# Performance work log

Hardware: AMD Instinct MI355X
Metric: run time of the kernel (lower is better)

## Reference

```python
import jax, jax.numpy as jnp
import numpy as np

B, Q, T, C = 2, 300, 25, 256
NH, NL, NP = 8, 4, 4
DFF = 1024
HD = C // NH
SHAPES = [(128, 128), (64, 64), (32, 32), (16, 16)]  # (H_l, W_l) per level
S = sum(h * w for h, w in SHAPES)
LQ = Q * T


def setup_inputs() -> dict:
    key = jax.random.key(0)
    ks = jax.random.split(key, 16)
    rn = lambda k, shape, s=0.02: jax.random.normal(k, shape, jnp.float32) * s
    starts = np.cumsum([0] + [h * w for h, w in SHAPES[:-1]])
    return {
        "tgt_text": jax.random.normal(ks[0], (B, Q, T, C), jnp.float32),
        "query_pos_text": jax.random.normal(ks[1], (B, Q, T, C), jnp.float32),
        "reference_points": jax.random.uniform(ks[2], (B, LQ, NL, 2), jnp.float32),
        "src": jax.random.normal(ks[3], (B, S, C), jnp.float32),
        "src_spatial_shapes": jnp.array(SHAPES, jnp.int32),
        "level_start_index": jnp.array(starts, jnp.int32),
        "in_proj_w": rn(ks[4], (3 * C, C)), "in_proj_b": jnp.zeros((3 * C,), jnp.float32),
        "out_proj_w": rn(ks[5], (C, C)), "out_proj_b": jnp.zeros((C,), jnp.float32),
        "ln1_g": jnp.ones((C,), jnp.float32), "ln1_b": jnp.zeros((C,), jnp.float32),
        "samp_off_w": rn(ks[6], (NH * NL * NP * 2, C)), "samp_off_b": rn(ks[7], (NH * NL * NP * 2,), 0.5),
        "aw_w": rn(ks[8], (NH * NL * NP, C)), "aw_b": jnp.zeros((NH * NL * NP,), jnp.float32),
        "vp_w": rn(ks[9], (C, C)), "vp_b": jnp.zeros((C,), jnp.float32),
        "op_w": rn(ks[10], (C, C)), "op_b": jnp.zeros((C,), jnp.float32),
        "ln2_g": jnp.ones((C,), jnp.float32), "ln2_b": jnp.zeros((C,), jnp.float32),
        "ffn1_w": rn(ks[11], (DFF, C)), "ffn1_b": jnp.zeros((DFF,), jnp.float32),
        "ffn2_w": rn(ks[12], (C, DFF)), "ffn2_b": jnp.zeros((C,), jnp.float32),
        "ln3_g": jnp.ones((C,), jnp.float32), "ln3_b": jnp.zeros((C,), jnp.float32),
    }


def _ln(x, g, b):
    m = jnp.mean(x, axis=-1, keepdims=True)
    v = jnp.var(x, axis=-1, keepdims=True)
    return (x - m) / jnp.sqrt(v + 1e-5) * g + b


def _self_attn(tgt, pos, in_proj_w, in_proj_b, out_proj_w, out_proj_b):
    # torch nn.MultiheadAttention math: q,k carry pos, v is raw tgt
    qk = (tgt + pos).reshape(B * Q, T, C)
    x = tgt.reshape(B * Q, T, C)
    Wq, Wk, Wv = jnp.split(in_proj_w, 3, axis=0)
    bq, bk, bv = jnp.split(in_proj_b, 3, axis=0)
    heads = lambda t: t.reshape(B * Q, T, NH, HD).transpose(0, 2, 1, 3)
    q = heads(qk @ Wq.T + bq)
    k = heads(qk @ Wk.T + bk)
    v = heads(x @ Wv.T + bv)
    attn = jax.nn.softmax(jnp.einsum("bhqd,bhkd->bhqk", q, k) / jnp.sqrt(jnp.float32(HD)), axis=-1)
    o = jnp.einsum("bhqk,bhkd->bhqd", attn, v).transpose(0, 2, 1, 3).reshape(B * Q, T, C)
    return (o @ out_proj_w.T + out_proj_b).reshape(B, Q, T, C)


def _ms_deform_attn(query, reference_points, src, shapes, samp_off_w, samp_off_b, aw_w, aw_b, vp_w, vp_b, op_w, op_b):
    # query: [B, LQ, C]; src: [B, S, C]
    value = (src @ vp_w.T + vp_b).reshape(B, S, NH, HD)
    off = (query @ samp_off_w.T + samp_off_b).reshape(B, LQ, NH, NL, NP, 2)
    aw = jax.nn.softmax((query @ aw_w.T + aw_b).reshape(B, LQ, NH, NL * NP), axis=-1)
    aw = aw.reshape(B, LQ, NH, NL, NP)
    # normalizer is (W_l, H_l)
    norm = jnp.array([[w, h] for (h, w) in shapes], jnp.float32)
    loc = reference_points[:, :, None, :, None, :] + off / norm[None, None, None, :, None, :]
    starts = np.cumsum([0] + [h * w for h, w in shapes])
    accum = jnp.zeros((B, NH, LQ, HD), jnp.float32)
    for l, (Hl, Wl) in enumerate(shapes):
        vl = value[:, starts[l]:starts[l] + Hl * Wl].transpose(0, 2, 1, 3)  # [B,NH,HW,HD]
        # grid_sample align_corners=False pixel coords
        xl = (loc[:, :, :, l, :, 0] * Wl - 0.5).transpose(0, 2, 1, 3).reshape(B, NH, LQ * NP)
        yl = (loc[:, :, :, l, :, 1] * Hl - 0.5).transpose(0, 2, 1, 3).reshape(B, NH, LQ * NP)
        x0 = jnp.floor(xl); y0 = jnp.floor(yl)
        wx1 = xl - x0; wy1 = yl - y0
        x0i = x0.astype(jnp.int32); y0i = y0.astype(jnp.int32)
        samp = jnp.zeros((B, NH, LQ * NP, HD), jnp.float32)
        for dx, dy, w in ((0, 0, (1 - wx1) * (1 - wy1)), (1, 0, wx1 * (1 - wy1)),
                          (0, 1, (1 - wx1) * wy1), (1, 1, wx1 * wy1)):
            xi = x0i + dx; yi = y0i + dy
            valid = (xi >= 0) & (xi < Wl) & (yi >= 0) & (yi < Hl)
            lin = jnp.clip(yi, 0, Hl - 1) * Wl + jnp.clip(xi, 0, Wl - 1)
            g = jnp.take_along_axis(vl, lin[..., None], axis=2)  # [B,NH,LQ*NP,HD]
            samp = samp + g * (w * valid)[..., None]
        samp = samp.reshape(B, NH, LQ, NP, HD)
        awl = aw[:, :, :, l, :].transpose(0, 2, 1, 3)  # [B,NH,LQ,NP]
        accum = accum + jnp.sum(samp * awl[..., None], axis=3)
    out = accum.transpose(0, 2, 1, 3).reshape(B, LQ, C)
    return out @ op_w.T + op_b


def reference(tgt_text, query_pos_text, reference_points, src, src_spatial_shapes, level_start_index,
              in_proj_w, in_proj_b, out_proj_w, out_proj_b, ln1_g, ln1_b,
              samp_off_w, samp_off_b, aw_w, aw_b, vp_w, vp_b, op_w, op_b, ln2_g, ln2_b,
              ffn1_w, ffn1_b, ffn2_w, ffn2_b, ln3_g, ln3_b):
    shapes = [tuple(int(v) for v in row) for row in np.asarray(src_spatial_shapes)]  # static
    # --- intra-text self-attention ---
    tgt2 = _self_attn(tgt_text, query_pos_text, in_proj_w, in_proj_b, out_proj_w, out_proj_b)
    tgt = _ln(tgt_text + tgt2, ln1_g, ln1_b)
    # --- multi-scale deformable cross-attention ---
    query = (tgt + query_pos_text).reshape(B, LQ, C)
    cross = _ms_deform_attn(query, reference_points, src, shapes,
                            samp_off_w, samp_off_b, aw_w, aw_b, vp_w, vp_b, op_w, op_b)
    tgt = _ln(tgt + cross.reshape(B, Q, T, C), ln2_g, ln2_b)
    # --- FFN ---
    ffn = jax.nn.relu(tgt @ ffn1_w.T + ffn1_b) @ ffn2_w.T + ffn2_b
    return _ln(tgt + ffn, ln3_g, ln3_b)
```

## Files before the change

### kernel.cpp

```cpp
#include <hip/hip_runtime.h>
#include <cstddef>

#define B_ 2
#define Q_ 300
#define T_ 25
#define C_ 256
#define NH_ 8
#define NL_ 4
#define NP_ 4
#define HD_ 32
#define DFF_ 1024
#define LQ_ (Q_ * T_)
#define NTOK_ (B_ * LQ_)
#define S_ 21760
#define BS_ (B_ * S_)

typedef __bf16 bf16x8 __attribute__((ext_vector_type(8)));
typedef float floatx4 __attribute__((ext_vector_type(4)));
typedef unsigned short ushort_t;

__device__ __forceinline__ unsigned pack_bf16(float x, float y) {
    unsigned ux = __float_as_uint(x) + 0x8000u;
    unsigned uy = __float_as_uint(y) + 0x8000u;
    return (ux >> 16) | (uy & 0xFFFF0000u);
}
__device__ __forceinline__ ushort_t f2bf_s(float x) {
    return (ushort_t)((__float_as_uint(x) + 0x8000u) >> 16);
}
__device__ __forceinline__ float bf2f(ushort_t u) {
    return __uint_as_float((unsigned)u << 16);
}

#define WOFF_IP   0
#define WOFF_OUT  196608
#define WOFF_VP   262144
#define WOFF_SO   327680
#define WOFF_AW   393216
#define WOFF_OP   425984
#define WOFF_F1   491520
#define WOFF_F2   753664
#define WTOTAL    1015808

__global__ __launch_bounds__(256) void convw_kernel(
    const float* __restrict__ ipw, const float* __restrict__ outw,
    const float* __restrict__ vpw, const float* __restrict__ sampw,
    const float* __restrict__ aww, const float* __restrict__ opw,
    const float* __restrict__ f1w, const float* __restrict__ f2w,
    ushort_t* __restrict__ dst)
{
    long long g = ((long long)blockIdx.x * 256 + threadIdx.x) * 8;
    if (g >= WTOTAL) return;
    const float* src; long long off;
    if      (g < WOFF_OUT) { src = ipw;   off = WOFF_IP; }
    else if (g < WOFF_VP)  { src = outw;  off = WOFF_OUT; }
    else if (g < WOFF_SO)  { src = vpw;   off = WOFF_VP; }
    else if (g < WOFF_AW)  { src = sampw; off = WOFF_SO; }
    else if (g < WOFF_OP)  { src = aww;   off = WOFF_AW; }
    else if (g < WOFF_F1)  { src = opw;   off = WOFF_OP; }
    else if (g < WOFF_F2)  { src = f1w;   off = WOFF_F1; }
    else                   { src = f2w;   off = WOFF_F2; }
    const float4* s4 = (const float4*)(src + (g - off));
    float4 a = s4[0], b = s4[1];
    uint4 o;
    o.x = pack_bf16(a.x, a.y); o.y = pack_bf16(a.z, a.w);
    o.z = pack_bf16(b.x, b.y); o.w = pack_bf16(b.z, b.w);
    *(uint4*)(dst + g) = o;
}

#define GBN 128
#define GBK 64
#define LDA_S 72

template<int AMODE, int OUTMODE, int GBMT>
__global__ __launch_bounds__(256) void gemm_w(
    const void* __restrict__ Av, const float* __restrict__ A2,
    const ushort_t* __restrict__ W,
    const float* __restrict__ bias, const float* __restrict__ bias2, int N1,
    void* __restrict__ Cv, long long partStride,
    int M, int N, int K, int kChunk, int ldc, int relu)
{
    constexpr int LA = GBMT / 16;
    constexpr int LB = 8;
    constexpr int WM = GBMT / 2;
    constexpr int NI = WM / 16;

    __shared__ unsigned short Asl[GBMT * LDA_S];
    __shared__ unsigned short Bsl[GBN * LDA_S];

    const int m0 = blockIdx.x * GBMT;
    if (m0 >= M) return;
    const int n0 = blockIdx.y * GBN;
    const int z  = blockIdx.z;
    const int kbeg = z * kChunk;
    const int kend = min(K, kbeg + kChunk);

    const int t  = threadIdx.x;
    const int wid  = t >> 6;
    const int lane = t & 63;
    const int wm = (wid >> 1) * WM;
    const int wn = (wid & 1) * 64;
    const int fm = lane & 15;
    const int fq = (lane >> 4) * 8;

    const bool addA2 = (AMODE == 1) && (n0 < N1);

    floatx4 acc[NI][4];
    #pragma unroll
    for (int i = 0; i < NI; ++i)
        #pragma unroll
        for (int j = 0; j < 4; ++j)
            acc[i][j] = (floatx4){0.f, 0.f, 0.f, 0.f};

    float4 pa[LA];
    uint2  pab[LA];
    uint2  pwb[LB];
    const float* Af = (const float*)Av;
    const ushort_t* Ab = (const ushort_t*)Av;

    auto load_tiles = [&](int k0) {
        #pragma unroll
        for (int i = 0; i < LA; ++i) {
            int idx = t + 256 * i;
            int row = idx >> 4;
            int c4  = (idx & 15) * 4;
            int gm = m0 + row;
            if constexpr (AMODE == 2) {
                uint2 v = {0u, 0u};
                if (gm < M) v = *(const uint2*)(Ab + (size_t)gm * K + k0 + c4);
                pab[i] = v;
            } else {
                float4 v = make_float4(0.f, 0.f, 0.f, 0.f);
                if (gm < M) {
                    v = *(const float4*)(Af + (size_t)gm * K + k0 + c4);
                    if constexpr (AMODE == 1) {
                        if (addA2) {
                            float4 v2 = *(const float4*)(A2 + (size_t)gm * K + k0 + c4);
                            v.x += v2.x; v.y += v2.y; v.z += v2.z; v.w += v2.w;
                        }
                    }
                }
                pa[i] = v;
            }
        }
        #pragma unroll
        for (int i = 0; i < LB; ++i) {
            int idx = t + 256 * i;
            int row = idx >> 4;
            int c4  = (idx & 15) * 4;
            pwb[i] = *(const uint2*)(W + (size_t)(n0 + row) * K + k0 + c4);
        }
    };

    load_tiles(kbeg);
    for (int k0 = kbeg; k0 < kend; k0 += GBK) {
        #pragma unroll
        for (int i = 0; i < LA; ++i) {
            int idx = t + 256 * i;
            int row = idx >> 4;
            int c4  = (idx & 15) * 4;
            if constexpr (AMODE == 2) {
                *(uint2*)&Asl[row * LDA_S + c4] = pab[i];
            } else {
                uint2 p;
                p.x = pack_bf16(pa[i].x, pa[i].y);
                p.y = pack_bf16(pa[i].z, pa[i].w);
                *(uint2*)&Asl[row * LDA_S + c4] = p;
            }
        }
        #pragma unroll
        for (int i = 0; i < LB; ++i) {
            int idx = t + 256 * i;
            int row = idx >> 4;
            int c4  = (idx & 15) * 4;
            *(uint2*)&Bsl[row * LDA_S + c4] = pwb[i];
        }
        if (k0 + GBK < kend) load_tiles(k0 + GBK);
        __syncthreads();

        #pragma unroll
        for (int kk = 0; kk < 2; ++kk) {
            bf16x8 af[NI], bfr[4];
            #pragma unroll
            for (int i = 0; i < NI; ++i)
                af[i] = *(const bf16x8*)&Asl[(wm + i * 16 + fm) * LDA_S + kk * 32 + fq];
            #pragma unroll
            for (int j = 0; j < 4; ++j)
                bfr[j] = *(const bf16x8*)&Bsl[(wn + j * 16 + fm) * LDA_S + kk * 32 + fq];

            #pragma unroll
            for (int i = 0; i < NI; ++i)
                #pragma unroll
                for (int j = 0; j < 4; ++j)
                    acc[i][j] = __builtin_amdgcn_mfma_f32_16x16x32_bf16(af[i], bfr[j], acc[i][j], 0, 0, 0);
        }
        __syncthreads();
    }

    float* Cf = (float*)Cv + (long long)z * partStride;
    ushort_t* Cb = (ushort_t*)Cv;
    const int cr = (lane >> 4) * 4;
    const int cc = lane & 15;
    #pragma unroll
    for (int j = 0; j < 4; ++j) {
        int gn = n0 + wn + j * 16 + cc;
        float bia = 0.f;
        if (z == 0) bia = (bias2 && gn >= N1) ? bias2[gn - N1] : bias[gn];
        #pragma unroll
        for (int i = 0; i < NI; ++i) {
            #pragma unroll
            for (int r = 0; r < 4; ++r) {
                int gm = m0 + wm + i * 16 + cr + r;
                if (gm < M) {
                    float v = acc[i][j][r] + bia;
                    if (relu) v = fmaxf(v, 0.f);
                    if constexpr (OUTMODE == 2) {
                        int bb = gm >= S_;
                        int s  = gm - bb * S_;
                        Cb[(((size_t)(bb * 8 + (gn >> 5))) * S_ + s) * 32 + (gn & 31)] = f2bf_s(v);
                    } else if constexpr (OUTMODE == 1) {
                        Cb[(size_t)gm * ldc + gn] = f2bf_s(v);
                    } else {
                        Cf[(size_t)gm * ldc + gn] = v;
                    }
                }
            }
        }
    }
}

__global__ __launch_bounds__(64) void attn_kernel(
    const ushort_t* __restrict__ qkv,
    ushort_t* __restrict__ o)
{
    int sh = blockIdx.x;
    int s = sh >> 3, h = sh & 7;
    __shared__ float qs[T_][HD_], ks[T_][HD_], vs[T_][HD_];
    int t = threadIdx.x;

    for (int idx = t; idx < T_ * HD_; idx += 64) {
        int i = idx >> 5, d = idx & 31;
        size_t base = ((size_t)(s * T_ + i)) * 768 + h * HD_ + d;
        qs[i][d] = bf2f(qkv[base]);
        ks[i][d] = bf2f(qkv[base + 256]);
        vs[i][d] = bf2f(qkv[base + 512]);
    }
    __syncthreads();

    if (t < T_) {
        float sc[T_];
        float mx = -1e30f;
        #pragma unroll
        for (int j = 0; j < T_; ++j) {
            float dot = 0.f;
            #pragma unroll
            for (int d = 0; d < HD_; ++d) dot += qs[t][d] * ks[j][d];
            sc[j] = dot * 0.17677669529663687f;
            mx = fmaxf(mx, sc[j]);
        }
        float sum = 0.f;
        #pragma unroll
        for (int j = 0; j < T_; ++j) { sc[j] = __expf(sc[j] - mx); sum += sc[j]; }
        float inv = 1.f / sum;
        float out[HD_];
        #pragma unroll
        for (int d = 0; d < HD_; ++d) out[d] = 0.f;
        for (int j = 0; j < T_; ++j) {
            float p = sc[j] * inv;
            #pragma unroll
            for (int d = 0; d < HD_; ++d) out[d] += p * vs[j][d];
        }
        size_t ob = ((size_t)(s * T_ + t)) * C_ + h * HD_;
        #pragma unroll
        for (int d = 0; d < HD_; ++d) o[ob + d] = f2bf_s(out[d]);
    }
}

__global__ __launch_bounds__(256) void ln4_kernel(
    const float* __restrict__ x, const float* __restrict__ r,
    int nparts, long long rstride,
    const float* __restrict__ g, const float* __restrict__ b,
    float* __restrict__ out, const float* __restrict__ pos,
    float* __restrict__ qout)
{
    const int wave = threadIdx.x >> 6;
    const int lane = threadIdx.x & 63;
    const int tok = blockIdx.x * 4 + wave;
    const size_t base = (size_t)tok * C_ + lane * 4;

    float4 v = *(const float4*)(x + base);
    for (int p = 0; p < nparts; ++p) {
        float4 rv = *(const float4*)(r + base + (long long)p * rstride);
        v.x += rv.x; v.y += rv.y; v.z += rv.z; v.w += rv.w;
    }
    float s  = v.x + v.y + v.z + v.w;
    float ss = v.x * v.x + v.y * v.y + v.z * v.z + v.w * v.w;
    #pragma unroll
    for (int m = 32; m; m >>= 1) {
        s  += __shfl_xor(s, m);
        ss += __shfl_xor(ss, m);
    }
    float mean = s * (1.f / 256.f);
    float var  = ss * (1.f / 256.f) - mean * mean;
    float rstd = rsqrtf(var + 1e-5f);

    float4 gv = *(const float4*)(g + lane * 4);
    float4 bv = *(const float4*)(b + lane * 4);
    float4 y;
    y.x = (v.x - mean) * rstd * gv.x + bv.x;
    y.y = (v.y - mean) * rstd * gv.y + bv.y;
    y.z = (v.z - mean) * rstd * gv.z + bv.z;
    y.w = (v.w - mean) * rstd * gv.w + bv.w;
    *(float4*)(out + base) = y;
    if (qout) {
        float4 pv = *(const float4*)(pos + base);
        float4 q;
        q.x = y.x + pv.x; q.y = y.y + pv.y; q.z = y.z + pv.z; q.w = y.w + pv.w;
        *(float4*)(qout + base) = q;
    }
}

#define DCHUNK_ 118
__global__ __launch_bounds__(256) void deform_kernel(
    const ushort_t* __restrict__ value,
    const float* __restrict__ d12,
    const float* __restrict__ refpts,
    ushort_t* __restrict__ out)
{
    const int bi    = blockIdx.x;
    const int xcd   = bi & 7;
    const int yy    = bi >> 3;
    const int combo = xcd + 8 * (yy & 1);
    const int chunk = yy >> 1;
    const int h     = combo & 7;
    const int b     = combo >> 3;

    __shared__ float tls[64][60];

    const int tid = threadIdx.x;
    const int t0  = chunk * 64;

    #pragma unroll
    for (int i = 0; i < 2; ++i) {
        int idx  = tid + 256 * i;
        int trow = idx >> 3;
        int c4   = (idx & 7) * 4;
        int tl   = min(t0 + trow, LQ_ - 1);
        float4 v;
        v.x = __builtin_nontemporal_load(d12 + (size_t)(b * LQ_ + tl) * 384 + h * 32 + c4 + 0);
        v.y = __builtin_nontemporal_load(d12 + (size_t)(b * LQ_ + tl) * 384 + h * 32 + c4 + 1);
        v.z = __builtin_nontemporal_load(d12 + (size_t)(b * LQ_ + tl) * 384 + h * 32 + c4 + 2);
        v.w = __builtin_nontemporal_load(d12 + (size_t)(b * LQ_ + tl) * 384 + h * 32 + c4 + 3);
        *(float4*)&tls[trow][c4] = v;
    }
    {
        int trow = tid >> 2;
        int c4   = (tid & 3) * 4;
        int tl   = min(t0 + trow, LQ_ - 1);
        float4 v;
        v.x = __builtin_nontemporal_load(d12 + (size_t)(b * LQ_ + tl) * 384 + 256 + h * 16 + c4 + 0);
        v.y = __builtin_nontemporal_load(d12 + (size_t)(b * LQ_ + tl) * 384 + 256 + h * 16 + c4 + 1);
        v.z = __builtin_nontemporal_load(d12 + (size_t)(b * LQ_ + tl) * 384 + 256 + h * 16 + c4 + 2);
        v.w = __builtin_nontemporal_load(d12 + (size_t)(b * LQ_ + tl) * 384 + 256 + h * 16 + c4 + 3);
        *(float4*)&tls[trow][32 + c4] = v;
    }
    if (tid < 128) {
        int trow = tid >> 1;
        int c4   = (tid & 1) * 4;
        int tl   = min(t0 + trow, LQ_ - 1);
        float4 v;
        v.x = __builtin_nontemporal_load(refpts + (size_t)(b * LQ_ + tl) * 8 + c4 + 0);
        v.y = __builtin_nontemporal_load(refpts + (size_t)(b * LQ_ + tl) * 8 + c4 + 1);
        v.z = __builtin_nontemporal_load(refpts + (size_t)(b * LQ_ + tl) * 8 + c4 + 2);
        v.w = __builtin_nontemporal_load(refpts + (size_t)(b * LQ_ + tl) * 8 + c4 + 3);
        *(float4*)&tls[trow][48 + c4] = v;
    }
    __syncthreads();

    if (tid < 64) {
        float lg[16];
        float mx = -1e30f;
        #pragma unroll
        for (int i = 0; i < 16; ++i) { lg[i] = tls[tid][32 + i]; mx = fmaxf(mx, lg[i]); }
        float sum = 0.f;
        #pragma unroll
        for (int i = 0; i < 16; ++i) { lg[i] = __expf(lg[i] - mx); sum += lg[i]; }
        float inv = 1.f / sum;
        #pragma unroll
        for (int i = 0; i < 16; ++i) tls[tid][32 + i] = lg[i] * inv;
    }
    __syncthreads();

    const int wave = tid >> 6;
    const int lane = tid & 63;
    const int ti   = lane >> 2;
    const int d8   = (lane & 3) * 8;
    const int row  = wave * 16 + ti;

    int tl = t0 + row;
    const bool active = (tl < LQ_);
    tl = min(tl, LQ_ - 1);
    const int tok = b * LQ_ + tl;

    const int HW[4]     = {128, 64, 32, 16};
    const int starts[4] = {0, 16384, 20480, 21504};

    const ushort_t* vplane = value + (size_t)combo * ((size_t)S_ * HD_) + d8;
    const float* trow = tls[row];

    float accv[8];
    #pragma unroll
    for (int i = 0; i < 8; ++i) accv[i] = 0.f;

    #pragma unroll
    for (int l = 0; l < 4; ++l) {
        const int Hl = HW[l], Wl = HW[l];
        float rx = trow[48 + l * 2 + 0];
        float ry = trow[48 + l * 2 + 1];
        const ushort_t* vbase = vplane + (size_t)starts[l] * HD_;
        #pragma unroll
        for (int p = 0; p < 4; ++p) {
            float ox = trow[l * 8 + p * 2 + 0];
            float oy = trow[l * 8 + p * 2 + 1];
            float aww = trow[32 + l * 4 + p];
            float xl = rx * (float)Wl + ox - 0.5f;
            float yl = ry * (float)Hl + oy - 0.5f;
            float x0f = floorf(xl), y0f = floorf(yl);
            int x0 = (int)x0f, y0 = (int)y0f;
            float wx1 = xl - x0f, wy1 = yl - y0f;
            float wx0 = 1.f - wx1, wy0 = 1.f - wy1;

            #pragma unroll
            for (int c = 0; c < 4; ++c) {
                int dx = c & 1, dy = c >> 1;
                int xi = x0 + dx, yi = y0 + dy;
                float w = (dx ? wx1 : wx0) * (dy ? wy1 : wy0);
                bool valid = (xi >= 0) & (xi < Wl) & (yi >= 0) & (yi < Hl);
                int xc = min(max(xi, 0), Wl - 1);
                int yc = min(max(yi, 0), Hl - 1);
                float wc = (valid ? w : 0.f) * aww;
                uint4 raw = *(const uint4*)(vbase + (size_t)(yc * Wl + xc) * HD_);
                accv[0] += __uint_as_float((raw.x & 0xFFFFu) << 16) * wc;
                accv[1] += __uint_as_float(raw.x & 0xFFFF0000u) * wc;
                accv[2] += __uint_as_float((raw.y & 0xFFFFu) << 16) * wc;
                accv[3] += __uint_as_float(raw.y & 0xFFFF0000u) * wc;
                accv[4] += __uint_as_float((raw.z & 0xFFFFu) << 16) * wc;
                accv[5] += __uint_as_float(raw.z & 0xFFFF0000u) * wc;
                accv[6] += __uint_as_float((raw.w & 0xFFFFu) << 16) * wc;
                accv[7] += __uint_as_float(raw.w & 0xFFFF0000u) * wc;
            }
        }
    }
    if (active) {
        uint4 po;
        po.x = pack_bf16(accv[0], accv[1]);
        po.y = pack_bf16(accv[2], accv[3]);
        po.z = pack_bf16(accv[4], accv[5]);
        po.w = pack_bf16(accv[6], accv[7]);
        *(uint4*)(out + (size_t)tok * C_ + h * HD_ + d8) = po;
    }
}

extern "C" void kernel_launch(void* const* d_in, const int* in_sizes, int n_in,
                              void* d_out, int out_size, void* d_ws, size_t ws_size,
                              hipStream_t stream) {
    const float* tgt_text = (const float*)d_in[0];
    const float* pos      = (const float*)d_in[1];
    const float* refpts   = (const float*)d_in[2];
    const float* src      = (const float*)d_in[3];
    const float* in_proj_w  = (const float*)d_in[6];
    const float* in_proj_b  = (const float*)d_in[7];
    const float* out_proj_w = (const float*)d_in[8];
    const float* out_proj_b = (const float*)d_in[9];
    const float* ln1_g = (const float*)d_in[10];
    const float* ln1_b = (const float*)d_in[11];
    const float* samp_off_w = (const float*)d_in[12];
    const float* samp_off_b = (const float*)d_in[13];
    const float* aw_w = (const float*)d_in[14];
    const float* aw_b = (const float*)d_in[15];
    const float* vp_w = (const float*)d_in[16];
    const float* vp_b = (const float*)d_in[17];
    const float* op_w = (const float*)d_in[18];
    const float* op_b = (const float*)d_in[19];
    const float* ln2_g = (const float*)d_in[20];
    const float* ln2_b = (const float*)d_in[21];
    const float* ffn1_w = (const float*)d_in[22];
    const float* ffn1_b = (const float*)d_in[23];
    const float* ffn2_w = (const float*)d_in[24];
    const float* ffn2_b = (const float*)d_in[25];
    const float* ln3_g = (const float*)d_in[26];
    const float* ln3_b = (const float*)d_in[27];

    const long long NC = (long long)NTOK_ * C_;
    float* ws = (float*)d_ws;
    float* A    = ws;
    float* Bq   = ws + NC;
    float* Creg = ws + 2 * NC;
    float* D12  = Creg + (long long)NTOK_ * DFF_;
    float* E    = D12 + (long long)NTOK_ * 384;
    float* F    = E + NC;
    ushort_t* wb = (ushort_t*)(F + NC);

    ushort_t* qkv  = (ushort_t*)Creg;
    ushort_t* valt = (ushort_t*)Creg + (size_t)NTOK_ * 768;

    const int MB64P  = 240;
    const int MB128P = 120;
    const int MBV64  = BS_ / 64;

    convw_kernel<<<496, 256, 0, stream>>>(in_proj_w, out_proj_w, vp_w, samp_off_w,
                                          aw_w, op_w, ffn1_w, ffn2_w, wb);
    gemm_w<1, 1, 64><<<dim3(MB64P, 6, 1), 256, 0, stream>>>(tgt_text, pos, wb + WOFF_IP,
        in_proj_b, nullptr, 512, qkv, 0, NTOK_, 768, 256, 256, 768, 0);
    gemm_w<0, 2, 64><<<dim3(MBV64, 2, 1), 256, 0, stream>>>(src, nullptr, wb + WOFF_VP,
        vp_b, nullptr, 0, valt, 0, BS_, 256, 256, 256, 0, 0);
    attn_kernel<<<B_ * Q_ * NH_, 64, 0, stream>>>(qkv, (ushort_t*)E);
    gemm_w<2, 0, 64><<<dim3(MB64P, 2, 1), 256, 0, stream>>>(E, nullptr, wb + WOFF_OUT,
        out_proj_b, nullptr, 0, F, 0, NTOK_, 256, 256, 256, 256, 0);
    ln4_kernel<<<NTOK_ / 4, 256, 0, stream>>>(tgt_text, F, 1, 0,
                                              ln1_g, ln1_b, A, pos, Bq);
    gemm_w<0, 0, 64><<<dim3(MB64P, 3, 1), 256, 0, stream>>>(Bq, nullptr, wb + WOFF_SO,
        samp_off_b, aw_b, 256, D12, 0, NTOK_, 384, 256, 256, 384, 0);
    deform_kernel<<<8 * 2 * DCHUNK_, 256, 0, stream>>>(valt, D12, refpts, (ushort_t*)E);
    gemm_w<2, 0, 64><<<dim3(MB64P, 2, 1), 256, 0, stream>>>(E, nullptr, wb + WOFF_OP,
        op_b, nullptr, 0, F, 0, NTOK_, 256, 256, 256, 256, 0);
    ln4_kernel<<<NTOK_ / 4, 256, 0, stream>>>(A, F, 1, 0,
                                              ln2_g, ln2_b, A, nullptr, nullptr);
    gemm_w<0, 1, 128><<<dim3(MB128P, 8, 1), 256, 0, stream>>>(A, nullptr, wb + WOFF_F1,
        ffn1_b, nullptr, 0, Creg, 0, NTOK_, DFF_, 256, 256, DFF_, 1);
    gemm_w<2, 0, 128><<<dim3(MB128P, 2, 2), 256, 0, stream>>>(Creg, nullptr, wb + WOFF_F2,
        ffn2_b, nullptr, 0, E, NC, NTOK_, 256, 1024, 512, 256, 0);
    ln4_kernel<<<NTOK_ / 4, 256, 0, stream>>>(A, E, 2, NC,
                                              ln3_g, ln3_b, (float*)d_out, nullptr, nullptr);
}
```

Before: 405.9 us.

## Stage bf16 GEMM epilogue through LDS and split-K the out-projection GEMMs

The bf16-output GEMM epilogues now write results into a per-wave shared-memory tile and then store full 16-byte rows, replacing scattered 2-byte global stores. The loop's barrier moves ahead of the next-tile prefetch. The two 256x256 projection GEMMs now use 2-way split-K into partial buffers, which the following layernorm kernel sums, so more blocks run concurrently. The price is extra partial-buffer traffic and workspace use, and restrict qualifiers are dropped on the layernorm kernel because its buffers may now alias.

```diff
diff --git a/kernel.cpp b/kernel.cpp
--- a/kernel.cpp
+++ b/kernel.cpp
@@ -84,8 +84,9 @@
     constexpr int WM = GBMT / 2;
     constexpr int NI = WM / 16;
 
-    __shared__ unsigned short Asl[GBMT * LDA_S];
-    __shared__ unsigned short Bsl[GBN * LDA_S];
+    __shared__ unsigned short SH[GBMT * LDA_S + GBN * LDA_S];
+    unsigned short* Asl = SH;
+    unsigned short* Bsl = SH + GBMT * LDA_S;
 
     const int m0 = blockIdx.x * GBMT;
     if (m0 >= M) return;
@@ -174,8 +175,8 @@
             int c4  = (idx & 15) * 4;
             *(uint2*)&Bsl[row * LDA_S + c4] = pwb[i];
         }
+        __syncthreads();
         if (k0 + GBK < kend) load_tiles(k0 + GBK);
-        __syncthreads();
 
         #pragma unroll
         for (int kk = 0; kk < 2; ++kk) {
@@ -200,28 +201,53 @@
     ushort_t* Cb = (ushort_t*)Cv;
     const int cr = (lane >> 4) * 4;
     const int cc = lane & 15;
-    #pragma unroll
-    for (int j = 0; j < 4; ++j) {
-        int gn = n0 + wn + j * 16 + cc;
-        float bia = 0.f;
-        if (z == 0) bia = (bias2 && gn >= N1) ? bias2[gn - N1] : bias[gn];
-        #pragma unroll
-        for (int i = 0; i < NI; ++i) {
-            #pragma unroll
-            for (int r = 0; r < 4; ++r) {
-                int gm = m0 + wm + i * 16 + cr + r;
-                if (gm < M) {
+
+    if constexpr (OUTMODE == 0) {
+        #pragma unroll
+        for (int j = 0; j < 4; ++j) {
+            int gn = n0 + wn + j * 16 + cc;
+            float bia = 0.f;
+            if (z == 0) bia = (bias2 && gn >= N1) ? bias2[gn - N1] : bias[gn];
+            #pragma unroll
+            for (int i = 0; i < NI; ++i)
+                #pragma unroll
+                for (int r = 0; r < 4; ++r) {
+                    int gm = m0 + wm + i * 16 + cr + r;
+                    if (gm < M) {
+                        float v = acc[i][j][r] + bia;
+                        if (relu) v = fmaxf(v, 0.f);
+                        Cf[(size_t)gm * ldc + gn] = v;
+                    }
+                }
+        }
+    } else {
+        unsigned short* epi = SH + wid * (WM * 64);
+        #pragma unroll
+        for (int j = 0; j < 4; ++j) {
+            int gn = n0 + wn + j * 16 + cc;
+            float bia = (bias2 && gn >= N1) ? bias2[gn - N1] : bias[gn];
+            #pragma unroll
+            for (int i = 0; i < NI; ++i)
+                #pragma unroll
+                for (int r = 0; r < 4; ++r) {
                     float v = acc[i][j][r] + bia;
                     if (relu) v = fmaxf(v, 0.f);
-                    if constexpr (OUTMODE == 2) {
-                        int bb = gm >= S_;
-                        int s  = gm - bb * S_;
-                        Cb[(((size_t)(bb * 8 + (gn >> 5))) * S_ + s) * 32 + (gn & 31)] = f2bf_s(v);
-                    } else if constexpr (OUTMODE == 1) {
-                        Cb[(size_t)gm * ldc + gn] = f2bf_s(v);
-                    } else {
-                        Cf[(size_t)gm * ldc + gn] = v;
-                    }
+                    epi[(i * 16 + cr + r) * 64 + j * 16 + cc] = f2bf_s(v);
+                }
+        }
+        #pragma unroll
+        for (int pass = 0; pass < WM / 8; ++pass) {
+            int lr = pass * 8 + (lane >> 3);
+            int gm = m0 + wm + lr;
+            uint4 vv = *(const uint4*)&epi[lr * 64 + (lane & 7) * 8];
+            if (gm < M) {
+                if constexpr (OUTMODE == 1) {
+                    *(uint4*)&Cb[(size_t)gm * ldc + n0 + wn + (lane & 7) * 8] = vv;
+                } else {
+                    int bb = gm >= S_;
+                    int s  = gm - bb * S_;
+                    int gh = n0 + wn + (lane & 7) * 8;
+                    *(uint4*)&Cb[(((size_t)(bb * 8 + (gh >> 5))) * S_ + s) * 32 + (gh & 31)] = vv;
                 }
             }
         }
@@ -276,11 +302,11 @@
 }
 
 __global__ __launch_bounds__(256) void ln4_kernel(
-    const float* __restrict__ x, const float* __restrict__ r,
+    const float* x, const float* r,
     int nparts, long long rstride,
     const float* __restrict__ g, const float* __restrict__ b,
-    float* __restrict__ out, const float* __restrict__ pos,
-    float* __restrict__ qout)
+    float* out, const float* __restrict__ pos,
+    float* qout)
 {
     const int wave = threadIdx.x >> 6;
     const int lane = threadIdx.x & 63;
@@ -514,16 +540,16 @@
     gemm_w<0, 2, 64><<<dim3(MBV64, 2, 1), 256, 0, stream>>>(src, nullptr, wb + WOFF_VP,
         vp_b, nullptr, 0, valt, 0, BS_, 256, 256, 256, 0, 0);
     attn_kernel<<<B_ * Q_ * NH_, 64, 0, stream>>>(qkv, (ushort_t*)E);
-    gemm_w<2, 0, 64><<<dim3(MB64P, 2, 1), 256, 0, stream>>>(E, nullptr, wb + WOFF_OUT,
-        out_proj_b, nullptr, 0, F, 0, NTOK_, 256, 256, 256, 256, 0);
-    ln4_kernel<<<NTOK_ / 4, 256, 0, stream>>>(tgt_text, F, 1, 0,
+    gemm_w<2, 0, 64><<<dim3(MB64P, 2, 2), 256, 0, stream>>>(E, nullptr, wb + WOFF_OUT,
+        out_proj_b, nullptr, 0, ws, NC, NTOK_, 256, 256, 128, 256, 0);
+    ln4_kernel<<<NTOK_ / 4, 256, 0, stream>>>(tgt_text, ws, 2, NC,
                                               ln1_g, ln1_b, A, pos, Bq);
     gemm_w<0, 0, 64><<<dim3(MB64P, 3, 1), 256, 0, stream>>>(Bq, nullptr, wb + WOFF_SO,
         samp_off_b, aw_b, 256, D12, 0, NTOK_, 384, 256, 256, 384, 0);
     deform_kernel<<<8 * 2 * DCHUNK_, 256, 0, stream>>>(valt, D12, refpts, (ushort_t*)E);
-    gemm_w<2, 0, 64><<<dim3(MB64P, 2, 1), 256, 0, stream>>>(E, nullptr, wb + WOFF_OP,
-        op_b, nullptr, 0, F, 0, NTOK_, 256, 256, 256, 256, 0);
-    ln4_kernel<<<NTOK_ / 4, 256, 0, stream>>>(A, F, 1, 0,
+    gemm_w<2, 0, 64><<<dim3(MB64P, 2, 2), 256, 0, stream>>>(E, nullptr, wb + WOFF_OP,
+        op_b, nullptr, 0, Creg, NC, NTOK_, 256, 256, 128, 256, 0);
+    ln4_kernel<<<NTOK_ / 4, 256, 0, stream>>>(A, Creg, 2, NC,
                                               ln2_g, ln2_b, A, nullptr, nullptr);
     gemm_w<0, 1, 128><<<dim3(MB128P, 8, 1), 256, 0, stream>>>(A, nullptr, wb + WOFF_F1,
         ffn1_b, nullptr, 0, Creg, 0, NTOK_, DFF_, 256, 256, DFF_, 1);
```

New measurement: 406.3 us. No clear change (+0.1%).
